# Kernel tuning notes

Hardware: AMD Instinct MI355X
Metric: run time of the kernel (lower is better)

Reference implementation:

```python
import jax, jax.numpy as jnp
import numpy as np

HIDDEN = 2048
N_HEADS = 16
N_KV = 4
HEAD_DIM = 128
SEQ = 2048
BATCH = 2
THETA = 10000.0


def rotate_half(x):
    half = x.shape[-1] // 2
    x1, x2 = x[..., :half], x[..., half:]
    return jnp.concatenate((-x2, x1), axis=-1)


def rope_cos_sin(seq_len, dim, theta, dtype):
    inv_freq = 1.0 / (theta ** (jnp.arange(0, dim, 2, dtype=jnp.float32) / dim))
    t = jnp.arange(seq_len, dtype=jnp.float32)
    freqs = jnp.einsum('i,j->ij', t, inv_freq)            # [S, dim/2]
    emb = jnp.concatenate((freqs, freqs), axis=-1)        # [S, dim]
    return jnp.cos(emb).astype(dtype), jnp.sin(emb).astype(dtype)


def setup_inputs() -> dict:
    key = jax.random.key(0)
    kx, kq, kk, kv, ko = jax.random.split(key, 5)
    s = 0.02
    return {
        'x':  jax.random.normal(kx, (BATCH, SEQ, HIDDEN), dtype=jnp.float32),
        'Wq': jax.random.normal(kq, (HIDDEN, N_HEADS * HEAD_DIM), dtype=jnp.float32) * s,
        'Wk': jax.random.normal(kk, (HIDDEN, N_KV * HEAD_DIM), dtype=jnp.float32) * s,
        'Wv': jax.random.normal(kv, (HIDDEN, N_KV * HEAD_DIM), dtype=jnp.float32) * s,
        'Wo': jax.random.normal(ko, (N_HEADS * HEAD_DIM, HIDDEN), dtype=jnp.float32) * s,
    }


def reference(x, Wq, Wk, Wv, Wo):
    B, S, _ = x.shape
    q = (x @ Wq).reshape(B, S, N_HEADS, HEAD_DIM)
    k = (x @ Wk).reshape(B, S, N_KV, HEAD_DIM)
    v = (x @ Wv).reshape(B, S, N_KV, HEAD_DIM)

    cos, sin = rope_cos_sin(S, HEAD_DIM, THETA, x.dtype)
    cos = cos[None, :, None, :]  # [1,S,1,D]
    sin = sin[None, :, None, :]
    q = q * cos + rotate_half(q) * sin
    k = k * cos + rotate_half(k) * sin

    repeat = N_HEADS // N_KV
    k = jnp.repeat(k, repeat, axis=2)  # repeat_interleave over heads
    v = jnp.repeat(v, repeat, axis=2)

    # [B,H,S,D]
    q = q.transpose(0, 2, 1, 3)
    k = k.transpose(0, 2, 1, 3)
    v = v.transpose(0, 2, 1, 3)

    scale = HEAD_DIM ** -0.5
    scores = jnp.einsum('bhqd,bhkd->bhqk', q, k) * scale
    causal = jnp.triu(jnp.full((S, S), -jnp.inf, dtype=scores.dtype), k=1)
    scores = scores + causal
    probs = jax.nn.softmax(scores, axis=-1)
    out = jnp.einsum('bhqk,bhkd->bhqd', probs, v)
    out = out.transpose(0, 2, 1, 3).reshape(B, S, N_HEADS * HEAD_DIM)
    return out @ Wo
```

## Files before the change

kernel.cpp:

```cpp
#include <hip/hip_runtime.h>
#include <hip/hip_bf16.h>
#include <math.h>

#define HIDDEN 2048
#define NHEADS 16
#define NKV 4
#define HD 128
#define SEQ 2048
#define BATCH 2
#define MTOT (BATCH*SEQ)
#define NQ (NHEADS*HD)
#define NKVD (NKV*HD)
#define NQKV (NQ + 2*NKVD)

typedef __attribute__((ext_vector_type(8))) short short8;
typedef __attribute__((ext_vector_type(4))) float float4v;

#if __has_builtin(__builtin_amdgcn_exp2f)
#define EXP2F __builtin_amdgcn_exp2f
#else
#define EXP2F exp2f
#endif
#define C1 0.1275174f

static __device__ __forceinline__ unsigned short f2bf(float f) {
  union { float f; unsigned int u; } v; v.f = f;
  unsigned int r = v.u + 0x7FFF + ((v.u >> 16) & 1);
  return (unsigned short)(r >> 16);
}
static __device__ __forceinline__ float bf2f(unsigned short h) {
  union { unsigned int u; float f; } v; v.u = ((unsigned int)h) << 16;
  return v.f;
}

static __device__ __forceinline__ void async16(const unsigned short* g, unsigned short* l) {
  __builtin_amdgcn_global_load_lds(
      (const __attribute__((address_space(1))) unsigned int*)g,
      (__attribute__((address_space(3))) unsigned int*)l, 16, 0, 0);
}

__global__ void cast_f32_bf16(const float* __restrict__ in,
                              unsigned short* __restrict__ out, int n) {
  int i = (blockIdx.x * blockDim.x + threadIdx.x) * 4;
  if (i < n) {
    float4 v = *(const float4*)(in + i);
    ushort4 o;
    o.x = f2bf(v.x); o.y = f2bf(v.y); o.z = f2bf(v.z); o.w = f2bf(v.w);
    *(ushort4*)(out + i) = o;
  }
}

__global__ void transpose_cast(const float* __restrict__ W,
                               unsigned short* __restrict__ Wt, int K, int N) {
  __shared__ float tile[32][33];
  int tn = blockIdx.x * 32;
  int tk = blockIdx.y * 32;
  int tx = threadIdx.x & 31;
  int ty = threadIdx.x >> 5;
  #pragma unroll
  for (int i = 0; i < 4; i++) {
    int k = tk + ty + i * 8;
    tile[ty + i * 8][tx] = W[(size_t)k * N + tn + tx];
  }
  __syncthreads();
  #pragma unroll
  for (int i = 0; i < 4; i++) {
    int n = tn + ty + i * 8;
    Wt[(size_t)n * K + tk + tx] = f2bf(tile[tx][ty + i * 8]);
  }
}

__global__ void rope_kernel(unsigned short* __restrict__ Qb, int nheads) {
  int idx = blockIdx.x * blockDim.x + threadIdx.x;
  int d = idx & 63;
  int hr = idx >> 6;
  int spos = (hr / nheads) % SEQ;
  size_t base = (size_t)hr * HD;
  float inv = exp2f((float)d * -0.2076205059304601f);
  float ang = (float)spos * inv;
  float sn, cs;
  sincosf(ang, &sn, &cs);
  float q1 = bf2f(Qb[base + d]);
  float q2 = bf2f(Qb[base + d + 64]);
  Qb[base + d]      = f2bf(q1 * cs - q2 * sn);
  Qb[base + d + 64] = f2bf(q2 * cs + q1 * sn);
}

__global__ __launch_bounds__(256) void gemm_qkv(
    const unsigned short* __restrict__ A,
    const unsigned short* __restrict__ Bt,
    unsigned short* __restrict__ Qb,
    unsigned short* __restrict__ Kb,
    unsigned short* __restrict__ Vt) {
  __shared__ unsigned short As0[128 * 32], Bs0[128 * 32];
  __shared__ unsigned short As1[128 * 32], Bs1[128 * 32];
  const int K = HIDDEN;
  int bm = blockIdx.y * 128, bn = blockIdx.x * 128;
  int tid = threadIdx.x, w = tid >> 6, lane = tid & 63;
  int wm = (w >> 1) * 64, wn = (w & 1) * 64;
  int m16 = lane & 15, quad = lane >> 4;
  int lrow = lane >> 2, lch = lane & 3;
  int lchs = lch ^ ((lrow >> 1) & 3);
  int qx = quad ^ ((m16 >> 1) & 3);
  const unsigned short* Ag = A + (size_t)(bm + w * 32 + lrow) * K + lchs * 8;
  const unsigned short* Bg = Bt + (size_t)(bn + w * 32 + lrow) * K + lchs * 8;
  int woff = w * 1024;

  float4v acc[4][4];
  #pragma unroll
  for (int i = 0; i < 4; i++)
    #pragma unroll
    for (int j = 0; j < 4; j++) acc[i][j] = (float4v)0.0f;

  auto stage = [&](int k0, unsigned short* Asl, unsigned short* Bsl) {
    #pragma unroll
    for (int i = 0; i < 2; i++) {
      async16(Ag + (size_t)i * 16 * K + k0, Asl + woff + i * 512);
      async16(Bg + (size_t)i * 16 * K + k0, Bsl + woff + i * 512);
    }
  };
  auto computeN = [&](const unsigned short* As, const unsigned short* Bs) {
    short8 af[4], bfr[4];
    #pragma unroll
    for (int i = 0; i < 4; i++)
      af[i] = *(const short8*)(&As[(wm + i * 16 + m16) * 32 + qx * 8]);
    #pragma unroll
    for (int j = 0; j < 4; j++)
      bfr[j] = *(const short8*)(&Bs[(wn + j * 16 + m16) * 32 + qx * 8]);
    #pragma unroll
    for (int i = 0; i < 4; i++)
      #pragma unroll
      for (int j = 0; j < 4; j++)
        acc[i][j] = __builtin_amdgcn_mfma_f32_16x16x32_bf16(af[i], bfr[j], acc[i][j], 0, 0, 0);
  };
  auto computeS = [&](const unsigned short* As, const unsigned short* Bs) {
    short8 af[4], bfr[4];
    #pragma unroll
    for (int i = 0; i < 4; i++)
      af[i] = *(const short8*)(&As[(wm + i * 16 + m16) * 32 + qx * 8]);
    #pragma unroll
    for (int j = 0; j < 4; j++)
      bfr[j] = *(const short8*)(&Bs[(wn + j * 16 + m16) * 32 + qx * 8]);
    #pragma unroll
    for (int i = 0; i < 4; i++)
      #pragma unroll
      for (int j = 0; j < 4; j++)
        acc[i][j] = __builtin_amdgcn_mfma_f32_16x16x32_bf16(bfr[j], af[i], acc[i][j], 0, 0, 0);
  };

  bool isV = (blockIdx.x >= 20);
  stage(0, As0, Bs0);
  if (!isV) {
    for (int k0 = 0; k0 < K; k0 += 64) {
      __syncthreads();
      if (k0 + 32 < K) stage(k0 + 32, As1, Bs1);
      computeN(As0, Bs0);
      __syncthreads();
      if (k0 + 64 < K) stage(k0 + 64, As0, Bs0);
      computeN(As1, Bs1);
    }
  } else {
    for (int k0 = 0; k0 < K; k0 += 64) {
      __syncthreads();
      if (k0 + 32 < K) stage(k0 + 32, As1, Bs1);
      computeS(As0, Bs0);
      __syncthreads();
      if (k0 + 64 < K) stage(k0 + 64, As0, Bs0);
      computeS(As1, Bs1);
    }
  }

  if (blockIdx.x < 16) {
    #pragma unroll
    for (int i = 0; i < 4; i++)
      #pragma unroll
      for (int j = 0; j < 4; j++)
        #pragma unroll
        for (int r = 0; r < 4; r++) {
          int row = bm + wm + i * 16 + quad * 4 + r;
          int col = bn + wn + j * 16 + m16;
          Qb[(size_t)row * NQ + col] = f2bf(acc[i][j][r]);
        }
  } else if (!isV) {
    #pragma unroll
    for (int i = 0; i < 4; i++)
      #pragma unroll
      for (int j = 0; j < 4; j++)
        #pragma unroll
        for (int r = 0; r < 4; r++) {
          int row = bm + wm + i * 16 + quad * 4 + r;
          int col = bn - 2048 + wn + j * 16 + m16;
          Kb[(size_t)row * NKVD + col] = f2bf(acc[i][j][r]);
        }
  } else {
    #pragma unroll
    for (int i = 0; i < 4; i++)
      #pragma unroll
      for (int j = 0; j < 4; j++)
        #pragma unroll
        for (int r = 0; r < 4; r++) {
          int f = bn - 2560 + wn + j * 16 + quad * 4 + r;
          int m = bm + wm + i * 16 + m16;
          Vt[(size_t)f * MTOT + m] = f2bf(acc[i][j][r]);
        }
  }
}

__global__ __launch_bounds__(256) void gemm_o(
    const unsigned short* __restrict__ A,
    const unsigned short* __restrict__ Bt,
    float* __restrict__ C, int M, int N, int K) {
  __shared__ unsigned short As0[128 * 32], Bs0[128 * 32];
  __shared__ unsigned short As1[128 * 32], Bs1[128 * 32];
  int bm = blockIdx.y * 128, bn = blockIdx.x * 128;
  int tid = threadIdx.x, w = tid >> 6, lane = tid & 63;
  int wm = (w >> 1) * 64, wn = (w & 1) * 64;
  int m16 = lane & 15, quad = lane >> 4;
  int lrow = lane >> 2, lch = lane & 3;
  int lchs = lch ^ ((lrow >> 1) & 3);
  int qx = quad ^ ((m16 >> 1) & 3);
  const unsigned short* Ag = A + (size_t)(bm + w * 32 + lrow) * K + lchs * 8;
  const unsigned short* Bg = Bt + (size_t)(bn + w * 32 + lrow) * K + lchs * 8;
  int woff = w * 1024;

  float4v acc[4][4];
  #pragma unroll
  for (int i = 0; i < 4; i++)
    #pragma unroll
    for (int j = 0; j < 4; j++) acc[i][j] = (float4v)0.0f;

  auto stage = [&](int k0, unsigned short* Asl, unsigned short* Bsl) {
    #pragma unroll
    for (int i = 0; i < 2; i++) {
      async16(Ag + (size_t)i * 16 * K + k0, Asl + woff + i * 512);
      async16(Bg + (size_t)i * 16 * K + k0, Bsl + woff + i * 512);
    }
  };
  auto compute = [&](const unsigned short* As, const unsigned short* Bs) {
    short8 af[4], bfr[4];
    #pragma unroll
    for (int i = 0; i < 4; i++)
      af[i] = *(const short8*)(&As[(wm + i * 16 + m16) * 32 + qx * 8]);
    #pragma unroll
    for (int j = 0; j < 4; j++)
      bfr[j] = *(const short8*)(&Bs[(wn + j * 16 + m16) * 32 + qx * 8]);
    #pragma unroll
    for (int i = 0; i < 4; i++)
      #pragma unroll
      for (int j = 0; j < 4; j++)
        acc[i][j] = __builtin_amdgcn_mfma_f32_16x16x32_bf16(af[i], bfr[j], acc[i][j], 0, 0, 0);
  };

  stage(0, As0, Bs0);
  for (int k0 = 0; k0 < K; k0 += 64) {
    __syncthreads();
    if (k0 + 32 < K) stage(k0 + 32, As1, Bs1);
    compute(As0, Bs0);
    __syncthreads();
    if (k0 + 64 < K) stage(k0 + 64, As0, Bs0);
    compute(As1, Bs1);
  }

  #pragma unroll
  for (int i = 0; i < 4; i++)
    #pragma unroll
    for (int j = 0; j < 4; j++)
      #pragma unroll
      for (int r = 0; r < 4; r++) {
        int row = bm + wm + i * 16 + quad * 4 + r;
        int col = bn + wn + j * 16 + m16;
        C[(size_t)row * N + col] = acc[i][j][r];
      }
}

#define FLASH_TILE(CUR, NXT)                                                  \
  {                                                                           \
    const int ktb = kt * 64;                                                  \
    __syncthreads();                                                 \
    {                                                                         \
      const unsigned short* Vg = Vt + vgrow * (size_t)MTOT                    \
                                    + (size_t)b * SEQ + ktb + kcv * 32 + vlch * 8; \
      unsigned short* Vl = Vs + kcv * 4096 + ipv * 512;                       \
      _Pragma("unroll")                                                       \
      for (int i = 0; i < 4; i++) async16(Vg + (size_t)i * 16 * MTOT, Vl + i * 512); \
    }                                                                         \
    const bool act = (ktb <= wqmax);                                          \
    float4v sacc[2][4];                                                       \
    if (act) {                                                                \
      _Pragma("unroll") for (int qs = 0; qs < 2; qs++)                        \
        _Pragma("unroll") for (int s4 = 0; s4 < 4; s4++) sacc[qs][s4] = (float4v)0.0f; \
      _Pragma("unroll")                                                       \
      for (int s4 = 0; s4 < 4; s4++)                                          \
        _Pragma("unroll")                                                     \
        for (int c = 0; c < 4; c++) {                                         \
          short8 kf = *(const short8*)(&CUR[c * 2048 + (s4 * 16 + m16) * 32 + qx * 8]); \
          sacc[0][s4] = __builtin_amdgcn_mfma_f32_16x16x32_bf16(kf, qf[0][c], sacc[0][s4], 0, 0, 0); \
          sacc[1][s4] = __builtin_amdgcn_mfma_f32_16x16x32_bf16(kf, qf[1][c], sacc[1][s4], 0, 0, 0); \
        }                                                                     \
    }                                                                         \
    if (kt < H) {                                                             \
      const unsigned short* Kg = Kp + (((size_t)b * SEQ + (kt + 1) * 64 + lrow) * NKV + kvh) * HD + w * 32 + vlch * 8; \
      unsigned short* Kl = NXT + w * 2048;                                    \
      _Pragma("unroll")                                                       \
      for (int i = 0; i < 4; i++) async16(Kg + (size_t)i * 16 * NKV * HD, Kl + i * 512); \
    }                                                                         \
    unsigned int pu[2][4][2];                                                 \
    if (act) {                                                                \
      _Pragma("unroll")                                                       \
      for (int qs = 0; qs < 2; qs++) {                                        \
        const int qabs = wqbase + qs * 16 + m16;                              \
        const bool diag = (ktb + 63) > (wqbase + qs * 16);                    \
        float sv[4][4]; float mloc = -1e30f;                                  \
        if (diag) {                                                           \
          _Pragma("unroll") for (int s4 = 0; s4 < 4; s4++)                    \
            _Pragma("unroll") for (int r = 0; r < 4; r++) {                   \
              int kabs = ktb + s4 * 16 + quad * 4 + r;                        \
              float t = sacc[qs][s4][r];                                      \
              sv[s4][r] = (kabs > qabs) ? -1e30f : t;                         \
              mloc = fmaxf(mloc, sv[s4][r]); }                                \
        } else {                                                              \
          _Pragma("unroll") for (int s4 = 0; s4 < 4; s4++)                    \
            _Pragma("unroll") for (int r = 0; r < 4; r++) {                   \
              sv[s4][r] = sacc[qs][s4][r]; mloc = fmaxf(mloc, sv[s4][r]); }   \
        }                                                                     \
        mloc *= C1;                                                           \
        mloc = fmaxf(mloc, __shfl_xor(mloc, 16, 64));                         \
        mloc = fmaxf(mloc, __shfl_xor(mloc, 32, 64));                         \
        const float mnewS = fmaxf(miS[qs], mloc);                             \
        float rs = 0.0f;                                                      \
        _Pragma("unroll") for (int s4 = 0; s4 < 4; s4++) {                    \
          float p0 = EXP2F(__builtin_fmaf(sv[s4][0], C1, -mnewS));            \
          float p1 = EXP2F(__builtin_fmaf(sv[s4][1], C1, -mnewS));            \
          float p2 = EXP2F(__builtin_fmaf(sv[s4][2], C1, -mnewS));            \
          float p3 = EXP2F(__builtin_fmaf(sv[s4][3], C1, -mnewS));            \
          rs += p0 + p1 + p2 + p3;                                            \
          pu[qs][s4][0] = (__float_as_uint(p1) & 0xffff0000u) | (__float_as_uint(p0) >> 16); \
          pu[qs][s4][1] = (__float_as_uint(p3) & 0xffff0000u) | (__float_as_uint(p2) >> 16); \
        }                                                                     \
        rs += __shfl_xor(rs, 16, 64);                                         \
        rs += __shfl_xor(rs, 32, 64);                                         \
        const float alpha = EXP2F(miS[qs] - mnewS);                           \
        li[qs] = li[qs] * alpha + rs; miS[qs] = mnewS;                        \
        _Pragma("unroll") for (int ds = 0; ds < 8; ds++) oacc[ds][qs] *= alpha; \
      }                                                                       \
    }                                                                         \
    __syncthreads();  \
    if (act) {                                                                \
      unsigned int* Pp = (unsigned int*)CUR;                                  \
      _Pragma("unroll")                                                       \
      for (int qs = 0; qs < 2; qs++) {                                        \
        const int prow = qlocal0 + qs * 16 + m16;                             \
        const int psw = prow * 32; const int rx = prow & 7;                   \
        _Pragma("unroll") for (int s4 = 0; s4 < 4; s4++) {                    \
          uint2 u; u.x = pu[qs][s4][0]; u.y = pu[qs][s4][1];                  \
          int chunkW = s4 * 2 + (quad >> 1);                                  \
          *(uint2*)(&Pp[psw + ((chunkW ^ rx) << 2) + (quad & 1) * 2]) = u;    \
        }                                                                     \
      }                                                                       \
      const int r0 = qlocal0 + m16, r1 = qlocal0 + 16 + m16;                  \
      _Pragma("unroll")                                                       \
      for (int kc = 0; kc < 2; kc++) {                                        \
        short8 pf0 = *(const short8*)(&Pp[r0 * 32 + (((kc * 4 + quad) ^ (r0 & 7)) << 2)]); \
        short8 pf1 = *(const short8*)(&Pp[r1 * 32 + (((kc * 4 + quad) ^ (r1 & 7)) << 2)]); \
        _Pragma("unroll")                                                     \
        for (int ds = 0; ds < 8; ds++) {                                      \
          short8 vf = *(const short8*)(&Vs[kc * 4096 + (ds * 16 + m16) * 32 + qx * 8]); \
          oacc[ds][0] = __builtin_amdgcn_mfma_f32_16x16x32_bf16(vf, pf0, oacc[ds][0], 0, 0, 0); \
          oacc[ds][1] = __builtin_amdgcn_mfma_f32_16x16x32_bf16(vf, pf1, oacc[ds][1], 0, 0, 0); \
        }                                                                     \
      }                                                                       \
    }                                                                         \
  }

__global__ __launch_bounds__(256, 2) void flash_attn(
    const unsigned short* __restrict__ Q,
    const unsigned short* __restrict__ Kp,
    const unsigned short* __restrict__ Vt,
    unsigned short* __restrict__ O) {
  __shared__ unsigned short Ks0[4 * 64 * 32];
  __shared__ unsigned short Ks1[4 * 64 * 32];
  __shared__ unsigned short Vs[2 * 128 * 32];

  int bx = blockIdx.x;
  int h  = blockIdx.y;
  int b  = blockIdx.z;
  int kvh = h >> 2;
  int H = 31 - bx, L = bx;
  int tid = threadIdx.x;
  int w = tid >> 6, lane = tid & 63;
  int m16 = lane & 15, quad = lane >> 4;
  int lrow = lane >> 2, lch = lane & 3;
  const int vlch = lch ^ ((lrow >> 1) & 3);
  const int qx = quad ^ ((m16 >> 1) & 3);

  int wqbase = (w < 2) ? (H * 64 + w * 32) : (L * 64 + (w - 2) * 32);
  int wqmax = wqbase + 31;
  int qlocal0 = w * 32;
  const int kcv = w >> 1, ipv = (w & 1) * 4;
  const size_t vgrow = (size_t)kvh * HD + ipv * 16 + lrow;

  short8 qf[2][4];
  #pragma unroll
  for (int qs = 0; qs < 2; qs++) {
    size_t qbase = (((size_t)b * SEQ + wqbase + qs * 16 + m16) * NHEADS + h) * HD;
    #pragma unroll
    for (int c = 0; c < 4; c++)
      qf[qs][c] = *(const short8*)(Q + qbase + c * 32 + quad * 8);
  }

  float4v oacc[8][2];
  #pragma unroll
  for (int ds = 0; ds < 8; ds++) { oacc[ds][0] = (float4v)0.0f; oacc[ds][1] = (float4v)0.0f; }
  float miS[2] = {-1e30f, -1e30f}, li[2] = {0.0f, 0.0f};

  {
    const unsigned short* Kg = Kp + (((size_t)b * SEQ + lrow) * NKV + kvh) * HD + w * 32 + vlch * 8;
    unsigned short* Kl = Ks0 + w * 2048;
    #pragma unroll
    for (int i = 0; i < 4; i++) async16(Kg + (size_t)i * 16 * NKV * HD, Kl + i * 512);
  }

  int kt = 0;
  for (;;) {
    FLASH_TILE(Ks0, Ks1)
    if (++kt > H) break;
    FLASH_TILE(Ks1, Ks0)
    if (++kt > H) break;
  }

  #pragma unroll
  for (int qs = 0; qs < 2; qs++) {
    float inv = 1.0f / li[qs];
    int qabs = wqbase + qs * 16 + m16;
    size_t obase = (((size_t)b * SEQ + qabs) * NHEADS + h) * HD + quad * 4;
    #pragma unroll
    for (int ds = 0; ds < 8; ds++) {
      float v0 = oacc[ds][qs][0] * inv;
      float v1 = oacc[ds][qs][1] * inv;
      float v2 = oacc[ds][qs][2] * inv;
      float v3 = oacc[ds][qs][3] * inv;
      uint2 u;
      u.x = ((unsigned)f2bf(v1) << 16) | f2bf(v0);
      u.y = ((unsigned)f2bf(v3) << 16) | f2bf(v2);
      *(uint2*)(O + obase + ds * 16) = u;
    }
  }
}

extern "C" void kernel_launch(void* const* d_in, const int* in_sizes, int n_in,
                              void* d_out, int out_size, void* d_ws, size_t ws_size,
                              hipStream_t stream) {
  const float* x  = (const float*)d_in[0];
  const float* Wq = (const float*)d_in[1];
  const float* Wk = (const float*)d_in[2];
  const float* Wv = (const float*)d_in[3];
  const float* Wo = (const float*)d_in[4];
  float* out = (float*)d_out;

  unsigned short* ws = (unsigned short*)d_ws;
  unsigned short* xb  = ws;
  unsigned short* Wqt = xb  + (size_t)MTOT * HIDDEN;
  unsigned short* Wkt = Wqt + (size_t)NQ * HIDDEN;
  unsigned short* Wvt = Wkt + (size_t)NKVD * HIDDEN;
  unsigned short* Wot = Wvt + (size_t)NKVD * HIDDEN;
  unsigned short* Qb  = Wot + (size_t)NQ * HIDDEN;
  unsigned short* Kb  = Qb  + (size_t)MTOT * NQ;
  unsigned short* Vtb = Kb  + (size_t)MTOT * NKVD;
  unsigned short* Ab  = Vtb + (size_t)MTOT * NKVD;

  cast_f32_bf16<<<(MTOT * HIDDEN / 4 + 255) / 256, 256, 0, stream>>>(x, xb, MTOT * HIDDEN);
  transpose_cast<<<dim3(NQ / 32, HIDDEN / 32), 256, 0, stream>>>(Wq, Wqt, HIDDEN, NQ);
  transpose_cast<<<dim3(NKVD / 32, HIDDEN / 32), 256, 0, stream>>>(Wk, Wkt, HIDDEN, NKVD);
  transpose_cast<<<dim3(NKVD / 32, HIDDEN / 32), 256, 0, stream>>>(Wv, Wvt, HIDDEN, NKVD);
  transpose_cast<<<dim3(NQ / 32, HIDDEN / 32), 256, 0, stream>>>(Wo, Wot, NQ, HIDDEN);

  gemm_qkv<<<dim3(NQKV / 128, MTOT / 128), 256, 0, stream>>>(xb, Wqt, Qb, Kb, Vtb);

  rope_kernel<<<(BATCH * SEQ * NHEADS * 64) / 256, 256, 0, stream>>>(Qb, NHEADS);
  rope_kernel<<<(BATCH * SEQ * NKV * 64) / 256, 256, 0, stream>>>(Kb, NKV);

  flash_attn<<<dim3(16, NHEADS, BATCH), 256, 0, stream>>>(Qb, Kb, Vtb, Ab);

  gemm_o<<<dim3(HIDDEN / 128, MTOT / 128), 256, 0, stream>>>(Ab, Wot, out, MTOT, HIDDEN, NQ);
}
```

Before: 340.9 us.

## Rebalance causal flash-attention work so each wave holds rows from both query tiles

Each of the four waves now owns 16 query rows from the high tile H and 16 from the low tile L, instead of whole 32-row halves of one tile. Every wave therefore stays busy through the whole key loop, and the late tiles (past L) run a single-query-set MFMA path. The P matrix is written straight to a dedicated shared buffer during softmax instead of being held in registers and copied into the K buffer after a barrier, and the next K tile prefetch is issued earlier. This adds shared memory, which may reduce occupancy, and adds divergent code paths.

```diff
diff --git a/kernel.cpp b/kernel.cpp
--- a/kernel.cpp
+++ b/kernel.cpp
@@ -276,7 +276,7 @@
 #define FLASH_TILE(CUR, NXT)                                                  \
   {                                                                           \
     const int ktb = kt * 64;                                                  \
-    __syncthreads();                                                 \
+    __syncthreads();        \
     {                                                                         \
       const unsigned short* Vg = Vt + vgrow * (size_t)MTOT                    \
                                     + (size_t)b * SEQ + ktb + kcv * 32 + vlch * 8; \
@@ -284,11 +284,17 @@
       _Pragma("unroll")                                                       \
       for (int i = 0; i < 4; i++) async16(Vg + (size_t)i * 16 * MTOT, Vl + i * 512); \
     }                                                                         \
-    const bool act = (ktb <= wqmax);                                          \
+    if (kt < H) {                                                             \
+      const unsigned short* Kg = Kp + (((size_t)b * SEQ + (kt + 1) * 64 + lrow) * NKV + kvh) * HD + w * 32 + vlch * 8; \
+      unsigned short* Kl = NXT + w * 2048;                                    \
+      _Pragma("unroll")                                                       \
+      for (int i = 0; i < 4; i++) async16(Kg + (size_t)i * 16 * NKV * HD, Kl + i * 512); \
+    }                                                                         \
+    const bool act1 = (ktb <= lmax_w);                                        \
     float4v sacc[2][4];                                                       \
-    if (act) {                                                                \
-      _Pragma("unroll") for (int qs = 0; qs < 2; qs++)                        \
-        _Pragma("unroll") for (int s4 = 0; s4 < 4; s4++) sacc[qs][s4] = (float4v)0.0f; \
+    _Pragma("unroll") for (int s4 = 0; s4 < 4; s4++) {                        \
+      sacc[0][s4] = (float4v)0.0f; sacc[1][s4] = (float4v)0.0f; }             \
+    if (act1) {                                                               \
       _Pragma("unroll")                                                       \
       for (int s4 = 0; s4 < 4; s4++)                                          \
         _Pragma("unroll")                                                     \
@@ -297,19 +303,21 @@
           sacc[0][s4] = __builtin_amdgcn_mfma_f32_16x16x32_bf16(kf, qf[0][c], sacc[0][s4], 0, 0, 0); \
           sacc[1][s4] = __builtin_amdgcn_mfma_f32_16x16x32_bf16(kf, qf[1][c], sacc[1][s4], 0, 0, 0); \
         }                                                                     \
+    } else {                                                                  \
+      _Pragma("unroll")                                                       \
+      for (int s4 = 0; s4 < 4; s4++)                                          \
+        _Pragma("unroll")                                                     \
+        for (int c = 0; c < 4; c++) {                                         \
+          short8 kf = *(const short8*)(&CUR[c * 2048 + (s4 * 16 + m16) * 32 + qx * 8]); \
+          sacc[0][s4] = __builtin_amdgcn_mfma_f32_16x16x32_bf16(kf, qf[0][c], sacc[0][s4], 0, 0, 0); \
+        }                                                                     \
     }                                                                         \
-    if (kt < H) {                                                             \
-      const unsigned short* Kg = Kp + (((size_t)b * SEQ + (kt + 1) * 64 + lrow) * NKV + kvh) * HD + w * 32 + vlch * 8; \
-      unsigned short* Kl = NXT + w * 2048;                                    \
-      _Pragma("unroll")                                                       \
-      for (int i = 0; i < 4; i++) async16(Kg + (size_t)i * 16 * NKV * HD, Kl + i * 512); \
-    }                                                                         \
-    unsigned int pu[2][4][2];                                                 \
-    if (act) {                                                                \
-      _Pragma("unroll")                                                       \
-      for (int qs = 0; qs < 2; qs++) {                                        \
-        const int qabs = wqbase + qs * 16 + m16;                              \
-        const bool diag = (ktb + 63) > (wqbase + qs * 16);                    \
+    _Pragma("unroll")                                                         \
+    for (int qs = 0; qs < 2; qs++) {                                          \
+      if (qs == 0 || act1) {                                                  \
+        const int tb = qs ? L : H;                                            \
+        const int qabs = tb * 64 + w * 16 + m16;                              \
+        const bool diag = (kt == tb);                                         \
         float sv[4][4]; float mloc = -1e30f;                                  \
         if (diag) {                                                           \
           _Pragma("unroll") for (int s4 = 0; s4 < 4; s4++)                    \
@@ -327,6 +335,8 @@
         mloc = fmaxf(mloc, __shfl_xor(mloc, 16, 64));                         \
         mloc = fmaxf(mloc, __shfl_xor(mloc, 32, 64));                         \
         const float mnewS = fmaxf(miS[qs], mloc);                             \
+        const int prow = qs * 64 + w * 16 + m16;                              \
+        const int psw = prow * 32; const int rx = prow & 7;                   \
         float rs = 0.0f;                                                      \
         _Pragma("unroll") for (int s4 = 0; s4 < 4; s4++) {                    \
           float p0 = EXP2F(__builtin_fmaf(sv[s4][0], C1, -mnewS));            \
@@ -334,8 +344,11 @@
           float p2 = EXP2F(__builtin_fmaf(sv[s4][2], C1, -mnewS));            \
           float p3 = EXP2F(__builtin_fmaf(sv[s4][3], C1, -mnewS));            \
           rs += p0 + p1 + p2 + p3;                                            \
-          pu[qs][s4][0] = (__float_as_uint(p1) & 0xffff0000u) | (__float_as_uint(p0) >> 16); \
-          pu[qs][s4][1] = (__float_as_uint(p3) & 0xffff0000u) | (__float_as_uint(p2) >> 16); \
+          uint2 u;                                                            \
+          u.x = (__float_as_uint(p1) & 0xffff0000u) | (__float_as_uint(p0) >> 16); \
+          u.y = (__float_as_uint(p3) & 0xffff0000u) | (__float_as_uint(p2) >> 16); \
+          int chunkW = s4 * 2 + (quad >> 1);                                  \
+          *(uint2*)(&Ps[psw + ((chunkW ^ rx) << 2) + (quad & 1) * 2]) = u;    \
         }                                                                     \
         rs += __shfl_xor(rs, 16, 64);                                         \
         rs += __shfl_xor(rs, 32, 64);                                         \
@@ -344,29 +357,30 @@
         _Pragma("unroll") for (int ds = 0; ds < 8; ds++) oacc[ds][qs] *= alpha; \
       }                                                                       \
     }                                                                         \
-    __syncthreads();  \
-    if (act) {                                                                \
-      unsigned int* Pp = (unsigned int*)CUR;                                  \
-      _Pragma("unroll")                                                       \
-      for (int qs = 0; qs < 2; qs++) {                                        \
-        const int prow = qlocal0 + qs * 16 + m16;                             \
-        const int psw = prow * 32; const int rx = prow & 7;                   \
-        _Pragma("unroll") for (int s4 = 0; s4 < 4; s4++) {                    \
-          uint2 u; u.x = pu[qs][s4][0]; u.y = pu[qs][s4][1];                  \
-          int chunkW = s4 * 2 + (quad >> 1);                                  \
-          *(uint2*)(&Pp[psw + ((chunkW ^ rx) << 2) + (quad & 1) * 2]) = u;    \
+    __syncthreads();     \
+    {                                                                         \
+      const int r0 = w * 16 + m16, r1 = 64 + w * 16 + m16;                    \
+      if (act1) {                                                             \
+        _Pragma("unroll")                                                     \
+        for (int kc = 0; kc < 2; kc++) {                                      \
+          short8 pf0 = *(const short8*)(&Ps[r0 * 32 + (((kc * 4 + quad) ^ (r0 & 7)) << 2)]); \
+          short8 pf1 = *(const short8*)(&Ps[r1 * 32 + (((kc * 4 + quad) ^ (r1 & 7)) << 2)]); \
+          _Pragma("unroll")                                                   \
+          for (int ds = 0; ds < 8; ds++) {                                    \
+            short8 vf = *(const short8*)(&Vs[kc * 4096 + (ds * 16 + m16) * 32 + qx * 8]); \
+            oacc[ds][0] = __builtin_amdgcn_mfma_f32_16x16x32_bf16(vf, pf0, oacc[ds][0], 0, 0, 0); \
+            oacc[ds][1] = __builtin_amdgcn_mfma_f32_16x16x32_bf16(vf, pf1, oacc[ds][1], 0, 0, 0); \
+          }                                                                   \
         }                                                                     \
-      }                                                                       \
-      const int r0 = qlocal0 + m16, r1 = qlocal0 + 16 + m16;                  \
-      _Pragma("unroll")                                                       \
-      for (int kc = 0; kc < 2; kc++) {                                        \
-        short8 pf0 = *(const short8*)(&Pp[r0 * 32 + (((kc * 4 + quad) ^ (r0 & 7)) << 2)]); \
-        short8 pf1 = *(const short8*)(&Pp[r1 * 32 + (((kc * 4 + quad) ^ (r1 & 7)) << 2)]); \
+      } else {                                                                \
         _Pragma("unroll")                                                     \
-        for (int ds = 0; ds < 8; ds++) {                                      \
-          short8 vf = *(const short8*)(&Vs[kc * 4096 + (ds * 16 + m16) * 32 + qx * 8]); \
-          oacc[ds][0] = __builtin_amdgcn_mfma_f32_16x16x32_bf16(vf, pf0, oacc[ds][0], 0, 0, 0); \
-          oacc[ds][1] = __builtin_amdgcn_mfma_f32_16x16x32_bf16(vf, pf1, oacc[ds][1], 0, 0, 0); \
+        for (int kc = 0; kc < 2; kc++) {                                      \
+          short8 pf0 = *(const short8*)(&Ps[r0 * 32 + (((kc * 4 + quad) ^ (r0 & 7)) << 2)]); \
+          _Pragma("unroll")                                                   \
+          for (int ds = 0; ds < 8; ds++) {                                    \
+            short8 vf = *(const short8*)(&Vs[kc * 4096 + (ds * 16 + m16) * 32 + qx * 8]); \
+            oacc[ds][0] = __builtin_amdgcn_mfma_f32_16x16x32_bf16(vf, pf0, oacc[ds][0], 0, 0, 0); \
+          }                                                                   \
         }                                                                     \
       }                                                                       \
     }                                                                         \
@@ -380,6 +394,7 @@
   __shared__ unsigned short Ks0[4 * 64 * 32];
   __shared__ unsigned short Ks1[4 * 64 * 32];
   __shared__ unsigned short Vs[2 * 128 * 32];
+  __shared__ unsigned int   Ps[128 * 32];
 
   int bx = blockIdx.x;
   int h  = blockIdx.y;
@@ -392,17 +407,18 @@
   int lrow = lane >> 2, lch = lane & 3;
   const int vlch = lch ^ ((lrow >> 1) & 3);
   const int qx = quad ^ ((m16 >> 1) & 3);
-
-  int wqbase = (w < 2) ? (H * 64 + w * 32) : (L * 64 + (w - 2) * 32);
-  int wqmax = wqbase + 31;
-  int qlocal0 = w * 32;
+  const int lmax_w = L * 64 + w * 16 + 15;
+
+  int qlocal0 = w * 16;
   const int kcv = w >> 1, ipv = (w & 1) * 4;
   const size_t vgrow = (size_t)kvh * HD + ipv * 16 + lrow;
+  (void)qlocal0;
 
   short8 qf[2][4];
   #pragma unroll
   for (int qs = 0; qs < 2; qs++) {
-    size_t qbase = (((size_t)b * SEQ + wqbase + qs * 16 + m16) * NHEADS + h) * HD;
+    int tb = qs ? L : H;
+    size_t qbase = (((size_t)b * SEQ + tb * 64 + w * 16 + m16) * NHEADS + h) * HD;
     #pragma unroll
     for (int c = 0; c < 4; c++)
       qf[qs][c] = *(const short8*)(Q + qbase + c * 32 + quad * 8);
@@ -431,7 +447,8 @@
   #pragma unroll
   for (int qs = 0; qs < 2; qs++) {
     float inv = 1.0f / li[qs];
-    int qabs = wqbase + qs * 16 + m16;
+    int tb = qs ? L : H;
+    int qabs = tb * 64 + w * 16 + m16;
     size_t obase = (((size_t)b * SEQ + qabs) * NHEADS + h) * HD + quad * 4;
     #pragma unroll
     for (int ds = 0; ds < 8; ds++) {
```

Result: faster. 311.6 us (-8.6%).
